# Kernel optimization log

Measured on AMD Instinct MI355X. Metric: run time of the kernel, lower is better.

## Reference

```python
import jax, jax.numpy as jnp
import numpy as np

VEC_DIM = 128   # D (also the per-head dim in this module)
HEADS = 8
PATCH = 4
WIN = 7
N_BATCH = 4
H_IMG = 448
W_IMG = 448


def _relative_index():
    # Swin-style relative position index, computed statically (matches torch code
    # which uses torch.meshgrid with default 'ij' indexing).
    coords = np.stack(np.meshgrid(np.arange(WIN), np.arange(WIN), indexing='ij'))  # [2,W,W]
    flat = coords.reshape(2, -1)                      # [2, W*W]
    rel = flat[:, :, None] - flat[:, None, :]         # [2, p, p]
    rel = rel.transpose(1, 2, 0).astype(np.int64)     # [p, p, 2]
    rel[:, :, 0] += WIN - 1
    rel[:, :, 1] += WIN - 1
    rel[:, :, 1] *= 2 * WIN - 1
    return rel.sum(-1)                                # [p, p], values in [0, (2W-1)^2)

REL_IDX = jnp.asarray(_relative_index())


def setup_inputs() -> dict:
    key = jax.random.key(0)
    ks = jax.random.split(key, 8)
    P = (H_IMG // PATCH) * (W_IMG // PATCH)  # 12544
    D, H = VEC_DIM, HEADS
    s = 0.02
    return {
        'x': jax.random.normal(ks[0], (N_BATCH, D, P), jnp.float32),
        'Wq': jax.random.normal(ks[1], (H * D, D), jnp.float32) * s,
        'bq': jnp.zeros((H * D,), jnp.float32),
        'Wk': jax.random.normal(ks[2], (H * D, D), jnp.float32) * s,
        'bk': jnp.zeros((H * D,), jnp.float32),
        'Wv': jax.random.normal(ks[3], (H * D, D), jnp.float32) * s,
        'bv': jnp.zeros((H * D,), jnp.float32),
        'Wo': jax.random.normal(ks[4], (D, H * D), jnp.float32) * s,
        'bo': jnp.zeros((D,), jnp.float32),
        'pos_code': jax.random.normal(ks[5], ((2 * WIN - 1) ** 2, H), jnp.float32) * s,
        'h': H_IMG,
        'w': W_IMG,
    }


def reference(x, Wq, bq, Wk, bk, Wv, bv, Wo, bo, pos_code, h, w):
    N, D, P = x.shape
    H = HEADS
    ch, cw = h // PATCH, w // PATCH
    nh, nw = ch // WIN, cw // WIN            # windows per axis
    p = WIN * WIN                            # tokens per window

    def emb(W, b):
        # pointwise Conv1d: [N,D,P] -> [N,H*D,P] -> [N,H,D,P]
        return (jnp.einsum('od,ndp->nop', W, x) + b[None, :, None]).reshape(N, H, D, P)

    def partition(e):
        # [N,H,D,P] -> [N,H,win_num,D,p]
        e = e.reshape(N, H, D, nh, WIN, nw, WIN)
        return e.transpose(0, 1, 3, 5, 2, 4, 6).reshape(N, H, nh * nw, D, p)

    q = partition(emb(Wq, bq))
    k = partition(emb(Wk, bk))
    v = partition(emb(Wv, bv))

    # attn[n,h,w,i,j] = sum_d k[n,h,w,d,i] * q[n,h,w,d,j], scaled
    attn = jnp.einsum('nhwdi,nhwdj->nhwij', k, q) / (D ** 0.5)
    bias = pos_code[REL_IDX].transpose(2, 0, 1)          # [H, p, p]
    attn = attn + bias[None, :, None, :, :]
    weights = jax.nn.softmax(attn, axis=3)               # softmax over key index i

    # out[n,h,w,d,j] = sum_i v[n,h,w,d,i] * weights[n,h,w,i,j]
    out = jnp.einsum('nhwdi,nhwij->nhwdj', v, weights)

    # window merge: [N,H,win_num,D,p] -> [N,H*D,P]
    out = out.reshape(N, H, nh, nw, D, WIN, WIN)
    out = out.transpose(0, 1, 4, 2, 5, 3, 6).reshape(N, H * D, P)

    return jnp.einsum('od,ndp->nop', Wo, out) + bo[None, :, None]
```

## Files before the change

kernel.cpp:

```cpp
#include <hip/hip_runtime.h>
#include <hip/hip_bf16.h>

typedef unsigned short u16;
typedef unsigned int u32;
typedef __attribute__((ext_vector_type(8))) short bf16x8;
typedef __attribute__((ext_vector_type(4))) float f32x4;
typedef __attribute__((ext_vector_type(2))) unsigned int u32x2;

#define NBATCH 4
#define DDIM   128
#define NHEAD  8
#define PTOT   12544
#define CWID   112
#define NTOK   49
#define PSTR   68
#define SCALE  0.08838834764831845f

#define OFF_US  6272
#define OFF_PL  14464
#define OFF_PCF 17796
#define OFF_CS  19148
#define LDS_TOT 20172

__device__ __forceinline__ float bf2f(u16 u) {
    union { u32 i; float f; } x; x.i = ((u32)u) << 16; return x.f;
}
__device__ __forceinline__ u16 f2bf(float f) {
    union { float f; u32 u; } v; v.f = f;
    return (u16)((v.u + 0x7fffu + ((v.u >> 16) & 1u)) >> 16);
}
__device__ __forceinline__ u32 pk2(float a, float b) {
    union { __hip_bfloat162 h; u32 u; } c;
    float2 t; t.x = a; t.y = b;
    c.h = __float22bfloat162_rn(t);
    return c.u;
}
__device__ __forceinline__ int swz128(int row, int col) {
    return row * 128 + ((((col >> 3) ^ (row & 15)) & 15) << 3) + (col & 7);
}

#define WS_WC   131072
#define WS_F32  262144

__global__ void __launch_bounds__(256) prep(
    const float* __restrict__ Wq, const float* __restrict__ Wk,
    const float* __restrict__ Wv, const float* __restrict__ Wo,
    const float* __restrict__ bq, const float* __restrict__ bk,
    const float* __restrict__ bv, u16* __restrict__ ws)
{
    __shared__ u16 lm[18432];
    const int tid = threadIdx.x;
    const int bb  = blockIdx.x;
    const int b   = bb >> 3;
    const int sub = bb & 7;
    const bool isG = (b >= 8);
    const int h = b & 7;
    const int r0 = sub * 16;
    float* fb = (float*)(ws + WS_F32);

    if (!isG) {
        for (int idx = tid; idx < 2048; idx += 256) {
            const int lr = idx >> 7, dh = idx & 127;
            lm[swz128(lr, dh)] = f2bf(Wo[(r0 + lr) * 1024 + h * 128 + dh]);
        }
        for (int idx = tid; idx < 16384; idx += 256) {
            const int dh = idx >> 7, d = idx & 127;
            lm[2048 + swz128(d, dh)] = f2bf(Wv[(h * 128 + dh) * 128 + d]);
        }
        if (sub == 0 && tid < 128) {
            float s = 0.f;
            for (int dh = 0; dh < 128; ++dh)
                s += Wo[tid * 1024 + h * 128 + dh] * bv[h * 128 + dh];
            fb[h * 128 + tid] = s;
        }
    } else {
        for (int idx = tid; idx < 2048; idx += 256) {
            const int dh = idx >> 4, lr = idx & 15;
            lm[swz128(lr, dh)] = f2bf(Wk[(h * 128 + dh) * 128 + r0 + lr]);
        }
        for (int idx = tid; idx < 16384; idx += 256) {
            const int dh = idx >> 7, dp = idx & 127;
            lm[2048 + swz128(dp, dh)] = f2bf(Wq[(h * 128 + dh) * 128 + dp]);
        }
        if (sub == 0 && tid < 128) {
            float r = 0.f, m = 0.f;
            for (int dh = 0; dh < 128; ++dh) {
                r += bk[h * 128 + dh] * Wq[(h * 128 + dh) * 128 + tid];
                m += Wk[(h * 128 + dh) * 128 + tid] * bq[h * 128 + dh];
            }
            fb[1024 + h * 128 + tid] = r * SCALE;
            fb[2048 + h * 128 + tid] = m * SCALE;
        }
        if (sub == 0 && tid == 0) {
            float s = 0.f;
            for (int dh = 0; dh < 128; ++dh) s += bk[h * 128 + dh] * bq[h * 128 + dh];
            fb[3072 + h] = s * SCALE;
        }
    }
    __syncthreads();

    const int w = tid >> 6, lane = tid & 63, quad = lane >> 4, lid = lane & 15;
    const f32x4 z4 = {0.f, 0.f, 0.f, 0.f};
    u16* dst = ws + (isG ? 0 : WS_WC) + h * 16384;
    const float gs = isG ? SCALE : 1.0f;
    bf16x8 A[4];
    #pragma unroll
    for (int kt = 0; kt < 4; ++kt)
        A[kt] = *(const bf16x8*)(lm + swz128(lid, kt * 32 + quad * 8));
    #pragma unroll
    for (int ntl = 0; ntl < 2; ++ntl) {
        const int nt = 2 * w + ntl;
        f32x4 acc = z4;
        #pragma unroll
        for (int kt = 0; kt < 4; ++kt) {
            bf16x8 B = *(const bf16x8*)(lm + 2048 + swz128(nt * 16 + lid, kt * 32 + quad * 8));
            acc = __builtin_amdgcn_mfma_f32_16x16x32_bf16(A[kt], B, acc, 0, 0, 0);
        }
        #pragma unroll
        for (int r = 0; r < 4; ++r) {
            const int row = r0 + quad * 4 + r, col = nt * 16 + lid;
            if (isG) dst[col * 128 + row] = f2bf(acc[r] * gs);
            else     dst[row * 128 + col] = f2bf(acc[r]);
        }
    }
}

__global__ void __launch_bounds__(256, 2)
winattn(const float* __restrict__ xg, const u16* __restrict__ ws,
        const float* __restrict__ bo, const float* __restrict__ posf,
        float* __restrict__ out)
{
    __shared__ __align__(16) u16 sm[LDS_TOT];
    u16* xw    = sm;
    u16* pl    = sm + OFF_PL;
    u16* pcf16 = sm + OFF_PCF;
    float* cs  = (float*)(sm + OFF_CS);

    const int tid  = threadIdx.x;
    const int w    = tid >> 6;
    const int lane = tid & 63;
    const int quad = lane >> 4;
    const int lid  = lane & 15;
    const int bx   = blockIdx.x;
    const int n    = bx >> 8;
    const int win  = bx & 255;
    const int pbase = (win >> 4) * 7 * CWID + (win & 15) * 7;

    const bf16x8 zf = {0,0,0,0,0,0,0,0};
    const f32x4  z4 = {0.f,0.f,0.f,0.f};

    const u16* Gt  = ws;
    const u16* Wcw = ws + WS_WC;
    const float* fb  = (const float*)(ws + WS_F32);
    const float* bcv = fb;
    const float* rP  = fb + 1024;
    const float* MP  = fb + 2048;
    const float* sP  = fb + 3072;

    for (int i = tid; i < 169 * NHEAD; i += 256) pcf16[i] = f2bf(posf[i]);
    const float* xn = xg + n * DDIM * PTOT;
    for (int idx = tid; idx < DDIM * NTOK; idx += 256) {
        int d = idx / NTOK;
        int t = idx - d * NTOK;
        int a = t / 7, b = t - a * 7;
        xw[swz128(t, d)] = f2bf(xn[d * PTOT + pbase + a * CWID + b]);
    }
    __syncthreads();

    bf16x8 xfrag[4][4];
    #pragma unroll
    for (int mt = 0; mt < 4; ++mt)
        #pragma unroll
        for (int kt = 0; kt < 4; ++kt)
            xfrag[mt][kt] = (mt * 16 + lid < NTOK)
                ? *(const bf16x8*)(xw + swz128(mt * 16 + lid, kt * 32 + quad * 8)) : zf;
    const int j = 16 * w + lid;
    bf16x8 xq[4];
    #pragma unroll
    for (int kt = 0; kt < 4; ++kt)
        xq[kt] = (j < NTOK)
            ? *(const bf16x8*)(xw + swz128(j, kt * 32 + quad * 8)) : zf;

    for (int hh = w; hh < NHEAD; hh += 4) {
        const float sh = sP[hh];
        #pragma unroll
        for (int mt = 0; mt < 4; ++mt) {
            float c = 0.f;
            #pragma unroll
            for (int kt = 0; kt < 4; ++kt)
                #pragma unroll
                for (int jj = 0; jj < 8; ++jj)
                    c += bf2f((u16)xfrag[mt][kt][jj]) * MP[hh * 128 + kt * 32 + quad * 8 + jj];
            c += __shfl_xor(c, 16);
            c += __shfl_xor(c, 32);
            if (quad == 0) cs[hh * 64 + mt * 16 + lid] = c + sh;
        }
    }
    __syncthreads();

    f32x4 outacc[8];
    #pragma unroll
    for (int nt = 0; nt < 8; ++nt) outacc[nt] = z4;

    const int jc = j < NTOK ? j : NTOK - 1;

    u16* tsb = sm;
    u16* usb = sm + OFF_US;

    for (int h = 0; h < NHEAD; ++h) {
        #pragma unroll
        for (int mtl = 0; mtl < 2; ++mtl) {
            const int mt = 2 * w + mtl;
            bf16x8 A[4];
            #pragma unroll
            for (int kt = 0; kt < 4; ++kt)
                A[kt] = *(const bf16x8*)(Gt + h * 16384 + (mt * 16 + lid) * 128 + kt * 32 + quad * 8);
            const f32x4 rb = *(const f32x4*)(rP + h * 128 + mt * 16 + quad * 4);
            const int dpb = mt * 16 + quad * 4;
            #pragma unroll
            for (int nt = 0; nt < 4; ++nt) {
                f32x4 acc = z4;
                #pragma unroll
                for (int kt = 0; kt < 4; ++kt)
                    acc = __builtin_amdgcn_mfma_f32_16x16x32_bf16(A[kt], xfrag[nt][kt], acc, 0, 0, 0);
                const int i = nt * 16 + lid;
                if (i < NTOK) {
                    u32x2 pkv;
                    pkv.x = pk2(acc[0] + rb[0], acc[1] + rb[1]);
                    pkv.y = pk2(acc[2] + rb[2], acc[3] + rb[3]);
                    *(u32x2*)(tsb + i * 128 + ((((dpb >> 3) ^ (i & 15)) & 15) << 3) + (dpb & 7)) = pkv;
                }
            }
        }
        #pragma unroll
        for (int ntl = 0; ntl < 2; ++ntl) {
            const int nt = 2 * w + ntl;
            bf16x8 B[4];
            #pragma unroll
            for (int kt = 0; kt < 4; ++kt)
                B[kt] = *(const bf16x8*)(Wcw + h * 16384 + (nt * 16 + lid) * 128 + kt * 32 + quad * 8);
            const int dd = nt * 16 + lid;
            const float bb = bcv[h * 128 + dd];
            #pragma unroll
            for (int mt = 0; mt < 4; ++mt) {
                f32x4 acc = z4;
                #pragma unroll
                for (int kt = 0; kt < 4; ++kt)
                    acc = __builtin_amdgcn_mfma_f32_16x16x32_bf16(xfrag[mt][kt], B[kt], acc, 0, 0, 0);
                const int ib = mt * 16 + quad * 4;
                u32x2 pkv;
                pkv.x = pk2(acc[0] + bb, acc[1] + bb);
                pkv.y = pk2(acc[2] + bb, acc[3] + bb);
                *(u32x2*)(usb + dd * 64 + ((((ib >> 3) ^ (dd & 7)) & 7) << 3) + (ib & 7)) = pkv;
            }
        }
        __syncthreads();

        f32x4 S[4];
        #pragma unroll
        for (int mt = 0; mt < 4; ++mt) {
            S[mt] = z4;
            #pragma unroll
            for (int kt = 0; kt < 4; ++kt) {
                bf16x8 A = *(const bf16x8*)(tsb + (mt * 16 + lid) * 128 + ((((kt * 4 + quad) ^ lid) & 15) << 3));
                S[mt] = __builtin_amdgcn_mfma_f32_16x16x32_bf16(A, xq[kt], S[mt], 0, 0, 0);
            }
        }
        const int aj = jc / 7, bj = jc - aj * 7;
        float sv[4][4];
        float mx = -3.0e38f;
        #pragma unroll
        for (int mt = 0; mt < 4; ++mt)
            #pragma unroll
            for (int r = 0; r < 4; ++r) {
                const int ii = mt * 16 + quad * 4 + r;
                float vvv;
                if (ii < NTOK) {
                    const int ai = ii / 7, bi = ii - ai * 7;
                    const int rel = (ai - aj + 6) + 13 * (bi - bj + 6);
                    vvv = S[mt][r] + cs[h * 64 + ii] + bf2f(pcf16[rel * NHEAD + h]);
                } else {
                    vvv = -3.0e38f;
                }
                sv[mt][r] = vvv;
                mx = fmaxf(mx, vvv);
            }
        mx = fmaxf(mx, __shfl_xor(mx, 16));
        mx = fmaxf(mx, __shfl_xor(mx, 32));
        float ssum = 0.f;
        #pragma unroll
        for (int mt = 0; mt < 4; ++mt)
            #pragma unroll
            for (int r = 0; r < 4; ++r) {
                const float e = __expf(sv[mt][r] - mx);
                sv[mt][r] = e;
                ssum += e;
            }
        ssum += __shfl_xor(ssum, 16);
        ssum += __shfl_xor(ssum, 32);
        const float inv = 1.0f / ssum;
        if (j < NTOK) {
            #pragma unroll
            for (int mt = 0; mt < 4; ++mt) {
                u32x2 pkv;
                pkv.x = pk2(sv[mt][0] * inv, sv[mt][1] * inv);
                pkv.y = pk2(sv[mt][2] * inv, sv[mt][3] * inv);
                *(u32x2*)(pl + j * PSTR + mt * 16 + quad * 4) = pkv;
            }
        }
        __threadfence_block();

        #pragma unroll
        for (int kt = 0; kt < 2; ++kt) {
            union { bf16x8 v; u32 u[4]; } Af;
            #pragma unroll
            for (int q2 = 0; q2 < 4; ++q2)
                Af.u[q2] = *(const u32*)(pl + jc * PSTR + kt * 32 + quad * 8 + 2 * q2);
            #pragma unroll
            for (int nt = 0; nt < 8; ++nt) {
                const int dd = nt * 16 + lid;
                bf16x8 Bu = *(const bf16x8*)(usb + dd * 64 + ((((kt * 4 + quad) ^ (dd & 7)) & 7) << 3));
                outacc[nt] = __builtin_amdgcn_mfma_f32_16x16x32_bf16(Af.v, Bu, outacc[nt], 0, 0, 0);
            }
        }
        if (h < NHEAD - 1) __syncthreads();
    }

    float* outp = out + n * DDIM * PTOT;
    #pragma unroll
    for (int nt = 0; nt < 8; ++nt) {
        const int dd = nt * 16 + lid;
        const float bov = bo[dd];
        #pragma unroll
        for (int r = 0; r < 4; ++r) {
            const int jj = 16 * w + quad * 4 + r;
            if (jj < NTOK) {
                const int a = jj / 7, b = jj - a * 7;
                outp[dd * PTOT + pbase + a * CWID + b] = outacc[nt][r] + bov;
            }
        }
    }
}

extern "C" void kernel_launch(void* const* d_in, const int* in_sizes, int n_in,
                              void* d_out, int out_size, void* d_ws, size_t ws_size,
                              hipStream_t stream) {
    (void)in_sizes; (void)n_in; (void)ws_size; (void)out_size;
    prep<<<128, 256, 0, stream>>>((const float*)d_in[1], (const float*)d_in[3],
                                  (const float*)d_in[5], (const float*)d_in[7],
                                  (const float*)d_in[2], (const float*)d_in[4],
                                  (const float*)d_in[6], (u16*)d_ws);
    winattn<<<NBATCH * 256, 256, 0, stream>>>(
        (const float*)d_in[0], (const u16*)d_ws,
        (const float*)d_in[8], (const float*)d_in[9], (float*)d_out);
}
```

Measured before the change: 236.4 us.

## Repartition projection work by token tile to cut registers and raise occupancy

Each wave now keeps only its own 16-token slice of x as fragments (4 instead of 16 bf16x8 registers) and loops over all 8 output tiles of the per-head projections, rather than holding every token tile and splitting by output tile. The column-sum precompute is reorganised the same way, and the launch bound goes from 2 to 3 blocks per SM. The aim is lower register pressure so more waves stay resident. In exchange each wave reloads all Gt/Wcw weight fragments from global memory per head, four times the previous weight traffic per block, and performs more VALU work on MP.

```diff
diff --git a/kernel.cpp b/kernel.cpp
--- a/kernel.cpp
+++ b/kernel.cpp
@@ -125,7 +125,7 @@
     }
 }
 
-__global__ void __launch_bounds__(256, 2)
+__global__ void __launch_bounds__(256, 3)
 winattn(const float* __restrict__ xg, const u16* __restrict__ ws,
         const float* __restrict__ bo, const float* __restrict__ posf,
         float* __restrict__ out)
@@ -167,34 +167,24 @@
     }
     __syncthreads();
 
-    bf16x8 xfrag[4][4];
-    #pragma unroll
-    for (int mt = 0; mt < 4; ++mt)
+    const int j = 16 * w + lid;
+    bf16x8 xfrag[4];
+    #pragma unroll
+    for (int kt = 0; kt < 4; ++kt)
+        xfrag[kt] = (j < NTOK)
+            ? *(const bf16x8*)(xw + swz128(j, kt * 32 + quad * 8)) : zf;
+
+    for (int hh = 0; hh < NHEAD; ++hh) {
+        const float sh = sP[hh];
+        float c = 0.f;
         #pragma unroll
         for (int kt = 0; kt < 4; ++kt)
-            xfrag[mt][kt] = (mt * 16 + lid < NTOK)
-                ? *(const bf16x8*)(xw + swz128(mt * 16 + lid, kt * 32 + quad * 8)) : zf;
-    const int j = 16 * w + lid;
-    bf16x8 xq[4];
-    #pragma unroll
-    for (int kt = 0; kt < 4; ++kt)
-        xq[kt] = (j < NTOK)
-            ? *(const bf16x8*)(xw + swz128(j, kt * 32 + quad * 8)) : zf;
-
-    for (int hh = w; hh < NHEAD; hh += 4) {
-        const float sh = sP[hh];
-        #pragma unroll
-        for (int mt = 0; mt < 4; ++mt) {
-            float c = 0.f;
-            #pragma unroll
-            for (int kt = 0; kt < 4; ++kt)
-                #pragma unroll
-                for (int jj = 0; jj < 8; ++jj)
-                    c += bf2f((u16)xfrag[mt][kt][jj]) * MP[hh * 128 + kt * 32 + quad * 8 + jj];
-            c += __shfl_xor(c, 16);
-            c += __shfl_xor(c, 32);
-            if (quad == 0) cs[hh * 64 + mt * 16 + lid] = c + sh;
-        }
+            #pragma unroll
+            for (int jj = 0; jj < 8; ++jj)
+                c += bf2f((u16)xfrag[kt][jj]) * MP[hh * 128 + kt * 32 + quad * 8 + jj];
+        c += __shfl_xor(c, 16);
+        c += __shfl_xor(c, 32);
+        if (quad == 0) cs[hh * 64 + 16 * w + lid] = c + sh;
     }
     __syncthreads();
 
@@ -203,51 +193,48 @@
     for (int nt = 0; nt < 8; ++nt) outacc[nt] = z4;
 
     const int jc = j < NTOK ? j : NTOK - 1;
+    const int aj = jc / 7, bj = jc - aj * 7;
 
     u16* tsb = sm;
     u16* usb = sm + OFF_US;
 
     for (int h = 0; h < NHEAD; ++h) {
-        #pragma unroll
-        for (int mtl = 0; mtl < 2; ++mtl) {
-            const int mt = 2 * w + mtl;
-            bf16x8 A[4];
-            #pragma unroll
-            for (int kt = 0; kt < 4; ++kt)
-                A[kt] = *(const bf16x8*)(Gt + h * 16384 + (mt * 16 + lid) * 128 + kt * 32 + quad * 8);
-            const f32x4 rb = *(const f32x4*)(rP + h * 128 + mt * 16 + quad * 4);
-            const int dpb = mt * 16 + quad * 4;
-            #pragma unroll
-            for (int nt = 0; nt < 4; ++nt) {
+        {
+            const int iT = 16 * w + lid;
+            #pragma unroll
+            for (int mt = 0; mt < 8; ++mt) {
+                bf16x8 A[4];
+                #pragma unroll
+                for (int kt = 0; kt < 4; ++kt)
+                    A[kt] = *(const bf16x8*)(Gt + h * 16384 + (mt * 16 + lid) * 128 + kt * 32 + quad * 8);
                 f32x4 acc = z4;
                 #pragma unroll
                 for (int kt = 0; kt < 4; ++kt)
-                    acc = __builtin_amdgcn_mfma_f32_16x16x32_bf16(A[kt], xfrag[nt][kt], acc, 0, 0, 0);
-                const int i = nt * 16 + lid;
-                if (i < NTOK) {
+                    acc = __builtin_amdgcn_mfma_f32_16x16x32_bf16(A[kt], xfrag[kt], acc, 0, 0, 0);
+                const int dpb = mt * 16 + quad * 4;
+                if (iT < NTOK) {
+                    const f32x4 rb = *(const f32x4*)(rP + h * 128 + dpb);
                     u32x2 pkv;
                     pkv.x = pk2(acc[0] + rb[0], acc[1] + rb[1]);
                     pkv.y = pk2(acc[2] + rb[2], acc[3] + rb[3]);
-                    *(u32x2*)(tsb + i * 128 + ((((dpb >> 3) ^ (i & 15)) & 15) << 3) + (dpb & 7)) = pkv;
+                    *(u32x2*)(tsb + iT * 128 + ((((dpb >> 3) ^ (iT & 15)) & 15) << 3) + (dpb & 7)) = pkv;
                 }
             }
         }
-        #pragma unroll
-        for (int ntl = 0; ntl < 2; ++ntl) {
-            const int nt = 2 * w + ntl;
-            bf16x8 B[4];
-            #pragma unroll
-            for (int kt = 0; kt < 4; ++kt)
-                B[kt] = *(const bf16x8*)(Wcw + h * 16384 + (nt * 16 + lid) * 128 + kt * 32 + quad * 8);
-            const int dd = nt * 16 + lid;
-            const float bb = bcv[h * 128 + dd];
-            #pragma unroll
-            for (int mt = 0; mt < 4; ++mt) {
+        {
+            const int ib = 16 * w + quad * 4;
+            #pragma unroll
+            for (int nt = 0; nt < 8; ++nt) {
+                bf16x8 B[4];
+                #pragma unroll
+                for (int kt = 0; kt < 4; ++kt)
+                    B[kt] = *(const bf16x8*)(Wcw + h * 16384 + (nt * 16 + lid) * 128 + kt * 32 + quad * 8);
                 f32x4 acc = z4;
                 #pragma unroll
                 for (int kt = 0; kt < 4; ++kt)
-                    acc = __builtin_amdgcn_mfma_f32_16x16x32_bf16(xfrag[mt][kt], B[kt], acc, 0, 0, 0);
-                const int ib = mt * 16 + quad * 4;
+                    acc = __builtin_amdgcn_mfma_f32_16x16x32_bf16(xfrag[kt], B[kt], acc, 0, 0, 0);
+                const int dd = nt * 16 + lid;
+                const float bb = bcv[h * 128 + dd];
                 u32x2 pkv;
                 pkv.x = pk2(acc[0] + bb, acc[1] + bb);
                 pkv.y = pk2(acc[2] + bb, acc[3] + bb);
@@ -262,11 +249,11 @@
             S[mt] = z4;
             #pragma unroll
             for (int kt = 0; kt < 4; ++kt) {
-                bf16x8 A = *(const bf16x8*)(tsb + (mt * 16 + lid) * 128 + ((((kt * 4 + quad) ^ lid) & 15) << 3));
-                S[mt] = __builtin_amdgcn_mfma_f32_16x16x32_bf16(A, xq[kt], S[mt], 0, 0, 0);
-            }
-        }
-        const int aj = jc / 7, bj = jc - aj * 7;
+                bf16x8 Abf = *(const bf16x8*)(tsb + (mt * 16 + lid) * 128 + ((((kt * 4 + quad) ^ lid) & 15) << 3));
+                S[mt] = __builtin_amdgcn_mfma_f32_16x16x32_bf16(Abf, xfrag[kt], S[mt], 0, 0, 0);
+            }
+        }
+
         float sv[4][4];
         float mx = -3.0e38f;
         #pragma unroll
```

Result: slower. 458.2 us (+93.8%).

## Warp-specialize window attention with producer/consumer waves and double-buffered per-head tiles

Applied to the files above, without the earlier changes.

Blocks grow to 512 threads. Four producer waves compute the next head's projected tiles into a double-buffered LDS area while four consumer waves run the scores, softmax and PV products for the current head. This leaves one barrier per head instead of two. The softmax drops max subtraction, and block indices are remapped so windows group by XCD. Register-held x fragments are replaced by repeated LDS reads. LDS use doubles, which may cut occupancy, and skipping the max subtraction risks overflow for large logits.

```diff
diff --git a/kernel.cpp b/kernel.cpp
--- a/kernel.cpp
+++ b/kernel.cpp
@@ -16,11 +16,13 @@
 #define PSTR   68
 #define SCALE  0.08838834764831845f
 
+#define BUFSZ   14464
 #define OFF_US  6272
-#define OFF_PL  14464
-#define OFF_PCF 17796
-#define OFF_CS  19148
-#define LDS_TOT 20172
+#define OFF_XW  28928
+#define OFF_PL  35200
+#define OFF_PCF 38532
+#define OFF_CS  39884
+#define LDS_TOT 40908
 
 __device__ __forceinline__ float bf2f(u16 u) {
     union { u32 i; float f; } x; x.i = ((u32)u) << 16; return x.f;
@@ -125,13 +127,13 @@
     }
 }
 
-__global__ void __launch_bounds__(256, 2)
+__global__ void __launch_bounds__(512, 4)
 winattn(const float* __restrict__ xg, const u16* __restrict__ ws,
         const float* __restrict__ bo, const float* __restrict__ posf,
         float* __restrict__ out)
 {
     __shared__ __align__(16) u16 sm[LDS_TOT];
-    u16* xw    = sm;
+    u16* xw    = sm + OFF_XW;
     u16* pl    = sm + OFF_PL;
     u16* pcf16 = sm + OFF_PCF;
     float* cs  = (float*)(sm + OFF_CS);
@@ -141,9 +143,11 @@
     const int lane = tid & 63;
     const int quad = lane >> 4;
     const int lid  = lane & 15;
-    const int bx   = blockIdx.x;
-    const int n    = bx >> 8;
-    const int win  = bx & 255;
+    const int bx0  = blockIdx.x;
+    const int xcd  = bx0 & 7;
+    const int idx0 = bx0 >> 3;
+    const int n    = idx0 >> 5;
+    const int win  = xcd * 32 + (idx0 & 31);
     const int pbase = (win >> 4) * 7 * CWID + (win & 15) * 7;
 
     const bf16x8 zf = {0,0,0,0,0,0,0,0};
@@ -157,9 +161,9 @@
     const float* MP  = fb + 2048;
     const float* sP  = fb + 3072;
 
-    for (int i = tid; i < 169 * NHEAD; i += 256) pcf16[i] = f2bf(posf[i]);
+    for (int i = tid; i < 169 * NHEAD; i += 512) pcf16[i] = f2bf(posf[i]);
     const float* xn = xg + n * DDIM * PTOT;
-    for (int idx = tid; idx < DDIM * NTOK; idx += 256) {
+    for (int idx = tid; idx < DDIM * NTOK; idx += 512) {
         int d = idx / NTOK;
         int t = idx - d * NTOK;
         int a = t / 7, b = t - a * 7;
@@ -167,64 +171,64 @@
     }
     __syncthreads();
 
-    bf16x8 xfrag[4][4];
-    #pragma unroll
-    for (int mt = 0; mt < 4; ++mt)
-        #pragma unroll
-        for (int kt = 0; kt < 4; ++kt)
-            xfrag[mt][kt] = (mt * 16 + lid < NTOK)
-                ? *(const bf16x8*)(xw + swz128(mt * 16 + lid, kt * 32 + quad * 8)) : zf;
-    const int j = 16 * w + lid;
-    bf16x8 xq[4];
-    #pragma unroll
-    for (int kt = 0; kt < 4; ++kt)
-        xq[kt] = (j < NTOK)
-            ? *(const bf16x8*)(xw + swz128(j, kt * 32 + quad * 8)) : zf;
-
-    for (int hh = w; hh < NHEAD; hh += 4) {
+    {
+        const int hh = w;
         const float sh = sP[hh];
         #pragma unroll
         for (int mt = 0; mt < 4; ++mt) {
             float c = 0.f;
             #pragma unroll
-            for (int kt = 0; kt < 4; ++kt)
+            for (int kt = 0; kt < 4; ++kt) {
+                bf16x8 xa = *(const bf16x8*)(xw + swz128(mt * 16 + lid, kt * 32 + quad * 8));
                 #pragma unroll
                 for (int jj = 0; jj < 8; ++jj)
-                    c += bf2f((u16)xfrag[mt][kt][jj]) * MP[hh * 128 + kt * 32 + quad * 8 + jj];
+                    c += bf2f((u16)xa[jj]) * MP[hh * 128 + kt * 32 + quad * 8 + jj];
+            }
             c += __shfl_xor(c, 16);
             c += __shfl_xor(c, 32);
             if (quad == 0) cs[hh * 64 + mt * 16 + lid] = c + sh;
         }
     }
-    __syncthreads();
-
+
+    const int j  = 16 * (w & 3) + lid;
+    const int jc = j < NTOK ? j : NTOK - 1;
+    const int aj = jc / 7, bj = jc - aj * 7;
+
+    bf16x8 xq[4];
     f32x4 outacc[8];
-    #pragma unroll
-    for (int nt = 0; nt < 8; ++nt) outacc[nt] = z4;
-
-    const int jc = j < NTOK ? j : NTOK - 1;
-
-    u16* tsb = sm;
-    u16* usb = sm + OFF_US;
-
-    for (int h = 0; h < NHEAD; ++h) {
-        #pragma unroll
-        for (int mtl = 0; mtl < 2; ++mtl) {
-            const int mt = 2 * w + mtl;
-            bf16x8 A[4];
+    if (w < 4) {
+        #pragma unroll
+        for (int kt = 0; kt < 4; ++kt)
+            xq[kt] = (j < NTOK)
+                ? *(const bf16x8*)(xw + swz128(j, kt * 32 + quad * 8)) : zf;
+        #pragma unroll
+        for (int nt = 0; nt < 8; ++nt) outacc[nt] = z4;
+    } else {
+        const int wp = w - 4;
+        u16* tsb = sm;
+        u16* usb = sm + OFF_US;
+        bf16x8 GA[2][4];
+        #pragma unroll
+        for (int mtl = 0; mtl < 2; ++mtl)
             #pragma unroll
             for (int kt = 0; kt < 4; ++kt)
-                A[kt] = *(const bf16x8*)(Gt + h * 16384 + (mt * 16 + lid) * 128 + kt * 32 + quad * 8);
-            const f32x4 rb = *(const f32x4*)(rP + h * 128 + mt * 16 + quad * 4);
-            const int dpb = mt * 16 + quad * 4;
-            #pragma unroll
-            for (int nt = 0; nt < 4; ++nt) {
+                GA[mtl][kt] = *(const bf16x8*)(Gt + ((2 * wp + mtl) * 16 + lid) * 128 + kt * 32 + quad * 8);
+        #pragma unroll
+        for (int nt = 0; nt < 4; ++nt) {
+            bf16x8 xb[4];
+            #pragma unroll
+            for (int kt = 0; kt < 4; ++kt)
+                xb[kt] = *(const bf16x8*)(xw + swz128(nt * 16 + lid, kt * 32 + quad * 8));
+            const int i = nt * 16 + lid;
+            #pragma unroll
+            for (int mtl = 0; mtl < 2; ++mtl) {
                 f32x4 acc = z4;
                 #pragma unroll
                 for (int kt = 0; kt < 4; ++kt)
-                    acc = __builtin_amdgcn_mfma_f32_16x16x32_bf16(A[kt], xfrag[nt][kt], acc, 0, 0, 0);
-                const int i = nt * 16 + lid;
+                    acc = __builtin_amdgcn_mfma_f32_16x16x32_bf16(GA[mtl][kt], xb[kt], acc, 0, 0, 0);
+                const int dpb = (2 * wp + mtl) * 16 + quad * 4;
                 if (i < NTOK) {
+                    const f32x4 rb = *(const f32x4*)(rP + dpb);
                     u32x2 pkv;
                     pkv.x = pk2(acc[0] + rb[0], acc[1] + rb[1]);
                     pkv.y = pk2(acc[2] + rb[2], acc[3] + rb[3]);
@@ -232,111 +236,184 @@
                 }
             }
         }
+        bf16x8 WB[2][4];
+        float bb[2];
         #pragma unroll
         for (int ntl = 0; ntl < 2; ++ntl) {
-            const int nt = 2 * w + ntl;
-            bf16x8 B[4];
             #pragma unroll
             for (int kt = 0; kt < 4; ++kt)
-                B[kt] = *(const bf16x8*)(Wcw + h * 16384 + (nt * 16 + lid) * 128 + kt * 32 + quad * 8);
+                WB[ntl][kt] = *(const bf16x8*)(Wcw + ((2 * wp + ntl) * 16 + lid) * 128 + kt * 32 + quad * 8);
+            bb[ntl] = bcv[(2 * wp + ntl) * 16 + lid];
+        }
+        #pragma unroll
+        for (int mt = 0; mt < 4; ++mt) {
+            bf16x8 xa[4];
+            #pragma unroll
+            for (int kt = 0; kt < 4; ++kt) {
+                bf16x8 v = *(const bf16x8*)(xw + swz128(mt * 16 + lid, kt * 32 + quad * 8));
+                xa[kt] = (mt < 3 || (mt * 16 + lid) < NTOK) ? v : zf;
+            }
+            const int ib = mt * 16 + quad * 4;
+            #pragma unroll
+            for (int ntl = 0; ntl < 2; ++ntl) {
+                f32x4 acc = z4;
+                #pragma unroll
+                for (int kt = 0; kt < 4; ++kt)
+                    acc = __builtin_amdgcn_mfma_f32_16x16x32_bf16(xa[kt], WB[ntl][kt], acc, 0, 0, 0);
+                const int dd = (2 * wp + ntl) * 16 + lid;
+                u32x2 pkv;
+                pkv.x = pk2(acc[0] + bb[ntl], acc[1] + bb[ntl]);
+                pkv.y = pk2(acc[2] + bb[ntl], acc[3] + bb[ntl]);
+                *(u32x2*)(usb + dd * 64 + ((((ib >> 3) ^ (dd & 7)) & 7) << 3) + (ib & 7)) = pkv;
+            }
+        }
+    }
+    __syncthreads();
+
+    for (int h = 0; h < NHEAD; ++h) {
+        if (w >= 4) {
+            if (h < NHEAD - 1) {
+                const int hn = h + 1;
+                const int wp = w - 4;
+                u16* tsb = sm + (hn & 1) * BUFSZ;
+                u16* usb = tsb + OFF_US;
+                bf16x8 GA[2][4];
+                #pragma unroll
+                for (int mtl = 0; mtl < 2; ++mtl)
+                    #pragma unroll
+                    for (int kt = 0; kt < 4; ++kt)
+                        GA[mtl][kt] = *(const bf16x8*)(Gt + hn * 16384 + ((2 * wp + mtl) * 16 + lid) * 128 + kt * 32 + quad * 8);
+                #pragma unroll
+                for (int nt = 0; nt < 4; ++nt) {
+                    bf16x8 xb[4];
+                    #pragma unroll
+                    for (int kt = 0; kt < 4; ++kt)
+                        xb[kt] = *(const bf16x8*)(xw + swz128(nt * 16 + lid, kt * 32 + quad * 8));
+                    const int i = nt * 16 + lid;
+                    #pragma unroll
+                    for (int mtl = 0; mtl < 2; ++mtl) {
+                        f32x4 acc = z4;
+                        #pragma unroll
+                        for (int kt = 0; kt < 4; ++kt)
+                            acc = __builtin_amdgcn_mfma_f32_16x16x32_bf16(GA[mtl][kt], xb[kt], acc, 0, 0, 0);
+                        const int dpb = (2 * wp + mtl) * 16 + quad * 4;
+                        if (i < NTOK) {
+                            const f32x4 rb = *(const f32x4*)(rP + hn * 128 + dpb);
+                            u32x2 pkv;
+                            pkv.x = pk2(acc[0] + rb[0], acc[1] + rb[1]);
+                            pkv.y = pk2(acc[2] + rb[2], acc[3] + rb[3]);
+                            *(u32x2*)(tsb + i * 128 + ((((dpb >> 3) ^ (i & 15)) & 15) << 3) + (dpb & 7)) = pkv;
+                        }
+                    }
+                }
+                bf16x8 WB[2][4];
+                float bb[2];
+                #pragma unroll
+                for (int ntl = 0; ntl < 2; ++ntl) {
+                    #pragma unroll
+                    for (int kt = 0; kt < 4; ++kt)
+                        WB[ntl][kt] = *(const bf16x8*)(Wcw + hn * 16384 + ((2 * wp + ntl) * 16 + lid) * 128 + kt * 32 + quad * 8);
+                    bb[ntl] = bcv[hn * 128 + (2 * wp + ntl) * 16 + lid];
+                }
+                #pragma unroll
+                for (int mt = 0; mt < 4; ++mt) {
+                    bf16x8 xa[4];
+                    #pragma unroll
+                    for (int kt = 0; kt < 4; ++kt) {
+                        bf16x8 v = *(const bf16x8*)(xw + swz128(mt * 16 + lid, kt * 32 + quad * 8));
+                        xa[kt] = (mt < 3 || (mt * 16 + lid) < NTOK) ? v : zf;
+                    }
+                    const int ib = mt * 16 + quad * 4;
+                    #pragma unroll
+                    for (int ntl = 0; ntl < 2; ++ntl) {
+                        f32x4 acc = z4;
+                        #pragma unroll
+                        for (int kt = 0; kt < 4; ++kt)
+                            acc = __builtin_amdgcn_mfma_f32_16x16x32_bf16(xa[kt], WB[ntl][kt], acc, 0, 0, 0);
+                        const int dd = (2 * wp + ntl) * 16 + lid;
+                        u32x2 pkv;
+                        pkv.x = pk2(acc[0] + bb[ntl], acc[1] + bb[ntl]);
+                        pkv.y = pk2(acc[2] + bb[ntl], acc[3] + bb[ntl]);
+                        *(u32x2*)(usb + dd * 64 + ((((ib >> 3) ^ (dd & 7)) & 7) << 3) + (ib & 7)) = pkv;
+                    }
+                }
+            }
+        } else {
+            u16* tsb = sm + (h & 1) * BUFSZ;
+            u16* usb = tsb + OFF_US;
+
+            f32x4 S[4];
+            #pragma unroll
+            for (int mt = 0; mt < 4; ++mt) {
+                S[mt] = z4;
+                #pragma unroll
+                for (int kt = 0; kt < 4; ++kt) {
+                    bf16x8 Abf = *(const bf16x8*)(tsb + (mt * 16 + lid) * 128 + ((((kt * 4 + quad) ^ lid) & 15) << 3));
+                    S[mt] = __builtin_amdgcn_mfma_f32_16x16x32_bf16(Abf, xq[kt], S[mt], 0, 0, 0);
+                }
+            }
+            float sv[4][4];
+            float ssum = 0.f;
+            #pragma unroll
+            for (int mt = 0; mt < 4; ++mt)
+                #pragma unroll
+                for (int r = 0; r < 4; ++r) {
+                    const int ii = mt * 16 + quad * 4 + r;
+                    float e;
+                    if (ii < NTOK) {
+                        const int ai = ii / 7, bi = ii - ai * 7;
+                        const int rel = (ai - aj + 6) + 13 * (bi - bj + 6);
+                        e = __expf(S[mt][r] + cs[h * 64 + ii] + bf2f(pcf16[rel * NHEAD + h]));
+                    } else {
+                        e = 0.0f;
+                    }
+                    sv[mt][r] = e;
+                    ssum += e;
+                }
+            ssum += __shfl_xor(ssum, 16);
+            ssum += __shfl_xor(ssum, 32);
+            const float inv = 1.0f / ssum;
+            if (j < NTOK) {
+                #pragma unroll
+                for (int mt = 0; mt < 4; ++mt) {
+                    u32x2 pkv;
+                    pkv.x = pk2(sv[mt][0] * inv, sv[mt][1] * inv);
+                    pkv.y = pk2(sv[mt][2] * inv, sv[mt][3] * inv);
+                    *(u32x2*)(pl + j * PSTR + mt * 16 + quad * 4) = pkv;
+                }
+            }
+            asm volatile("s_waitcnt lgkmcnt(0)" ::: "memory");
+
+            #pragma unroll
+            for (int kt = 0; kt < 2; ++kt) {
+                union { bf16x8 v; u32 u[4]; } Af;
+                #pragma unroll
+                for (int q2 = 0; q2 < 4; ++q2)
+                    Af.u[q2] = *(const u32*)(pl + jc * PSTR + kt * 32 + quad * 8 + 2 * q2);
+                #pragma unroll
+                for (int nt = 0; nt < 8; ++nt) {
+                    const int dd = nt * 16 + lid;
+                    bf16x8 Bu = *(const bf16x8*)(usb + dd * 64 + ((((kt * 4 + quad) ^ (dd & 7)) & 7) << 3));
+                    outacc[nt] = __builtin_amdgcn_mfma_f32_16x16x32_bf16(Af.v, Bu, outacc[nt], 0, 0, 0);
+                }
+            }
+        }
+        __syncthreads();
+    }
+
+    if (w < 4) {
+        float* outp = out + n * DDIM * PTOT;
+        #pragma unroll
+        for (int nt = 0; nt < 8; ++nt) {
             const int dd = nt * 16 + lid;
-            const float bb = bcv[h * 128 + dd];
-            #pragma unroll
-            for (int mt = 0; mt < 4; ++mt) {
-                f32x4 acc = z4;
-                #pragma unroll
-                for (int kt = 0; kt < 4; ++kt)
-                    acc = __builtin_amdgcn_mfma_f32_16x16x32_bf16(xfrag[mt][kt], B[kt], acc, 0, 0, 0);
-                const int ib = mt * 16 + quad * 4;
-                u32x2 pkv;
-                pkv.x = pk2(acc[0] + bb, acc[1] + bb);
-                pkv.y = pk2(acc[2] + bb, acc[3] + bb);
-                *(u32x2*)(usb + dd * 64 + ((((ib >> 3) ^ (dd & 7)) & 7) << 3) + (ib & 7)) = pkv;
-            }
-        }
-        __syncthreads();
-
-        f32x4 S[4];
-        #pragma unroll
-        for (int mt = 0; mt < 4; ++mt) {
-            S[mt] = z4;
-            #pragma unroll
-            for (int kt = 0; kt < 4; ++kt) {
-                bf16x8 A = *(const bf16x8*)(tsb + (mt * 16 + lid) * 128 + ((((kt * 4 + quad) ^ lid) & 15) << 3));
-                S[mt] = __builtin_amdgcn_mfma_f32_16x16x32_bf16(A, xq[kt], S[mt], 0, 0, 0);
-            }
-        }
-        const int aj = jc / 7, bj = jc - aj * 7;
-        float sv[4][4];
-        float mx = -3.0e38f;
-        #pragma unroll
-        for (int mt = 0; mt < 4; ++mt)
+            const float bov = bo[dd];
             #pragma unroll
             for (int r = 0; r < 4; ++r) {
-                const int ii = mt * 16 + quad * 4 + r;
-                float vvv;
-                if (ii < NTOK) {
-                    const int ai = ii / 7, bi = ii - ai * 7;
-                    const int rel = (ai - aj + 6) + 13 * (bi - bj + 6);
-                    vvv = S[mt][r] + cs[h * 64 + ii] + bf2f(pcf16[rel * NHEAD + h]);
-                } else {
-                    vvv = -3.0e38f;
-                }
-                sv[mt][r] = vvv;
-                mx = fmaxf(mx, vvv);
-            }
-        mx = fmaxf(mx, __shfl_xor(mx, 16));
-        mx = fmaxf(mx, __shfl_xor(mx, 32));
-        float ssum = 0.f;
-        #pragma unroll
-        for (int mt = 0; mt < 4; ++mt)
-            #pragma unroll
-            for (int r = 0; r < 4; ++r) {
-                const float e = __expf(sv[mt][r] - mx);
-                sv[mt][r] = e;
-                ssum += e;
-            }
-        ssum += __shfl_xor(ssum, 16);
-        ssum += __shfl_xor(ssum, 32);
-        const float inv = 1.0f / ssum;
-        if (j < NTOK) {
-            #pragma unroll
-            for (int mt = 0; mt < 4; ++mt) {
-                u32x2 pkv;
-                pkv.x = pk2(sv[mt][0] * inv, sv[mt][1] * inv);
-                pkv.y = pk2(sv[mt][2] * inv, sv[mt][3] * inv);
-                *(u32x2*)(pl + j * PSTR + mt * 16 + quad * 4) = pkv;
-            }
-        }
-        __threadfence_block();
-
-        #pragma unroll
-        for (int kt = 0; kt < 2; ++kt) {
-            union { bf16x8 v; u32 u[4]; } Af;
-            #pragma unroll
-            for (int q2 = 0; q2 < 4; ++q2)
-                Af.u[q2] = *(const u32*)(pl + jc * PSTR + kt * 32 + quad * 8 + 2 * q2);
-            #pragma unroll
-            for (int nt = 0; nt < 8; ++nt) {
-                const int dd = nt * 16 + lid;
-                bf16x8 Bu = *(const bf16x8*)(usb + dd * 64 + ((((kt * 4 + quad) ^ (dd & 7)) & 7) << 3));
-                outacc[nt] = __builtin_amdgcn_mfma_f32_16x16x32_bf16(Af.v, Bu, outacc[nt], 0, 0, 0);
-            }
-        }
-        if (h < NHEAD - 1) __syncthreads();
-    }
-
-    float* outp = out + n * DDIM * PTOT;
-    #pragma unroll
-    for (int nt = 0; nt < 8; ++nt) {
-        const int dd = nt * 16 + lid;
-        const float bov = bo[dd];
-        #pragma unroll
-        for (int r = 0; r < 4; ++r) {
-            const int jj = 16 * w + quad * 4 + r;
-            if (jj < NTOK) {
-                const int a = jj / 7, b = jj - a * 7;
-                outp[dd * PTOT + pbase + a * CWID + b] = outacc[nt][r] + bov;
+                const int jj = 16 * (w & 3) + quad * 4 + r;
+                if (jj < NTOK) {
+                    const int a = jj / 7, b = jj - a * 7;
+                    outp[dd * PTOT + pbase + a * CWID + b] = outacc[nt][r] + bov;
+                }
             }
         }
     }
@@ -350,7 +427,7 @@
                                   (const float*)d_in[5], (const float*)d_in[7],
                                   (const float*)d_in[2], (const float*)d_in[4],
                                   (const float*)d_in[6], (u16*)d_ws);
-    winattn<<<NBATCH * 256, 256, 0, stream>>>(
+    winattn<<<NBATCH * 256, 512, 0, stream>>>(
         (const float*)d_in[0], (const u16*)d_ws,
         (const float*)d_in[8], (const float*)d_in[9], (float*)d_out);
 }
```

Result: slower. 316.2 us (+33.8%).
